# Kernel tuning notes

Measured on AMD Instinct MI355X. Metric: run time of the kernel, lower is better.

The kernel has to match this reference:

```python
import jax, jax.numpy as jnp
import numpy as np

B, C, H, W = 4096, 2, 64, 64
D = 1.0 / (H - 1)  # grid spacing d0 = d1
CLAMP_MIN = -27.6310211159


def fd1_last(f, d):
    # 2nd-order accurate first derivative along last axis, non-periodic.
    c = (f[..., 2:] - f[..., :-2]) / (2.0 * d)
    lo = (-3.0 * f[..., 0:1] + 4.0 * f[..., 1:2] - f[..., 2:3]) / (2.0 * d)
    hi = (3.0 * f[..., -1:] - 4.0 * f[..., -2:-1] + f[..., -3:-2]) / (2.0 * d)
    return jnp.concatenate([lo, c, hi], axis=-1)


def fd2_last(f, d):
    # 2nd-order accurate second derivative along last axis, non-periodic.
    d2 = d * d
    c = (f[..., 2:] - 2.0 * f[..., 1:-1] + f[..., :-2]) / d2
    lo = (2.0 * f[..., 0:1] - 5.0 * f[..., 1:2] + 4.0 * f[..., 2:3] - f[..., 3:4]) / d2
    hi = (2.0 * f[..., -1:] - 5.0 * f[..., -2:-1] + 4.0 * f[..., -3:-2] - f[..., -4:-3]) / d2
    return jnp.concatenate([lo, c, hi], axis=-1)


def fd_axis(f, d, axis, order):
    fn = fd1_last if order == 1 else fd2_last
    if axis == -1 or axis == f.ndim - 1:
        return fn(f, d)
    g = jnp.swapaxes(f, axis, -1)
    return jnp.swapaxes(fn(g, d), axis, -1)


def darcy_source(h, w, r=10.0, w_frac=0.125):
    ww = int(round(w_frac * h))
    f = np.zeros((h, w), dtype=np.float32)
    f[:ww, :ww] = r
    f[-ww:, -ww:] = -r
    return jnp.asarray(f)


def compute_residual(x0):
    # x0: (B, 2, H, W) with channel 0 = pressure p, channel 1 = permeability K
    p, perm = x0[:, 0], x0[:, 1]
    p_d0 = fd_axis(p, D, -2, 1)
    p_d1 = fd_axis(p, D, -1, 1)
    p_d00 = fd_axis(p, D, -2, 2)
    p_d11 = fd_axis(p, D, -1, 2)
    perm_d0 = fd_axis(perm, D, -2, 1)
    perm_d1 = fd_axis(perm, D, -1, 1)

    f_s = darcy_source(H, W)  # (H, W)
    # div(-K grad p) - f  (only diagonal of velocity jacobian is populated)
    eq0 = (-perm * p_d00 - perm_d0 * p_d0) + (-perm * p_d11 - perm_d1 * p_d1) - f_s  # (B,H,W)

    # Neumann boundary residuals on grad p (channel 0 = d/d0, channel 1 = d/d1)
    bc = jnp.zeros((x0.shape[0], 2, H, W), dtype=x0.dtype)
    bc = bc.at[:, 0, 0, :].set(-p_d0[:, 0, :])
    bc = bc.at[:, 0, -1, :].set(p_d0[:, -1, :])
    bc = bc.at[:, 1, :, 0].set(p_d1[:, :, 0])
    bc = bc.at[:, 1, :, -1].set(-p_d1[:, :, -1])

    # b c x y -> b (x y) c  layout, then concat eq0 as an extra channel
    eq0_flat = eq0.reshape(eq0.shape[0], H * W, 1)
    bc_flat = jnp.transpose(bc, (0, 2, 3, 1)).reshape(bc.shape[0], H * W, 2)
    residual = jnp.concatenate([eq0_flat, bc_flat], axis=-1)  # (B, HW, 3)
    return residual.mean(axis=(1, 2))  # (B,)


def darcy_loss(model_out, target, x0_hat, var):
    data_loss = jnp.mean((model_out - target) ** 2)
    r = compute_residual(x0_hat)  # (B,)
    ll = -0.5 * (r ** 2) / var  # gaussian log-likelihood of 0 under N(r, var)
    ll = jnp.maximum(ll, CLAMP_MIN)
    residual_loss = jnp.mean(-ll)
    c_residual = 1.0
    return data_loss + c_residual * residual_loss


def setup_inputs() -> dict:
    key = jax.random.key(0)
    k1, k2, k3, k4 = jax.random.split(key, 4)
    return {
        "model_out": jax.random.normal(k1, (B, C, H, W), dtype=jnp.float32),
        "target": jax.random.normal(k2, (B, C, H, W), dtype=jnp.float32),
        "x0_hat": jax.random.normal(k3, (B, C, H, W), dtype=jnp.float32),
        "var": jax.random.uniform(k4, (B,), dtype=jnp.float32, minval=0.5, maxval=1.5),
    }


def reference(model_out, target, x0_hat, var):
    return darcy_loss(model_out, target, x0_hat, var)
```

## Files before the change

### kernel.cpp

```cpp
#include <hip/hip_runtime.h>


#define NB 4096
#define HW 4096
#define CHW 8192

__device__ __forceinline__ void hderiv2(float v, int j, float& d1, float& d11) {
    constexpr float INV2D = 31.5f, INVD2 = 3969.0f;
    float vm = __shfl(v, (j + 63) & 63);
    float vp = __shfl(v, (j + 1) & 63);
    float v2 = __shfl(v, (j == 0) ? 2 : 61);
    float v3 = __shfl(v, (j == 0) ? 3 : 60);
    d1  = (vp - vm) * INV2D;
    d11 = (vp - 2.0f * v + vm) * INVD2;
    if (j == 0)  { d1 = (-3.0f * v + 4.0f * vp - v2) * INV2D;
                   d11 = (2.0f * v - 5.0f * vp + 4.0f * v2 - v3) * INVD2; }
    if (j == 63) { d1 = ( 3.0f * v - 4.0f * vm + v2) * INV2D;
                   d11 = (2.0f * v - 5.0f * vm + 4.0f * v2 - v3) * INVD2; }
}

__device__ __forceinline__ float hderiv1(float v, int j) {
    constexpr float INV2D = 31.5f;
    float vm = __shfl(v, (j + 63) & 63);
    float vp = __shfl(v, (j + 1) & 63);
    float v2 = __shfl(v, (j == 0) ? 2 : 61);
    float d = (vp - vm) * INV2D;
    if (j == 0)  d = (-3.0f * v + 4.0f * vp - v2) * INV2D;
    if (j == 63) d = ( 3.0f * v - 4.0f * vm + v2) * INV2D;
    return d;
}

__global__ __launch_bounds__(256, 8) void darcy_wave_kernel(
    const float* __restrict__ mo, const float* __restrict__ tg,
    const float* __restrict__ x0, const float* __restrict__ var,
    float* __restrict__ ws_res, float* __restrict__ ws_data)
{
    constexpr float INV2D = 31.5f;
    constexpr float INVD2 = 3969.0f;
    constexpr float CLAMP = 27.6310211159f;

    const int wave = threadIdx.x >> 6;
    const int j    = threadIdx.x & 63;
    const int b    = blockIdx.x * 4 + wave;

    const float*  pb = x0 + (size_t)b * CHW;
    const float*  qb = pb + HW;
    const float4* m4 = (const float4*)(mo + (size_t)b * CHW);
    const float4* g4 = (const float4*)(tg + (size_t)b * CHW);

    float rsum = 0.0f, dsum = 0.0f;

    float pm = pb[j], pc = pb[64 + j], pp = pb[128 + j], pn = pb[192 + j];
    float qm = qb[j], qc = qb[64 + j], qp = qb[128 + j], qn = qb[192 + j];

    {
        float pd1, pd11;
        hderiv2(pm, j, pd1, pd11);
        float qd1 = hderiv1(qm, j);
        float pd0  = (-3.0f * pm + 4.0f * pc - pp) * INV2D;
        float pd00 = (2.0f * pm - 5.0f * pc + 4.0f * pp - pn) * INVD2;
        float qd0  = (-3.0f * qm + 4.0f * qc - qp) * INV2D;
        rsum += -qm * (pd00 + pd11) - qd0 * pd0 - qd1 * pd1 - pd0;
        rsum += (j == 0) ? pd1 : 0.0f;
        rsum -= (j == 63) ? pd1 : 0.0f;
    }

    float s_p60 = 0.0f, s_p61 = 0.0f, s_q61 = 0.0f;

    #pragma unroll 2
    for (int i = 1; i <= 62; ++i) {
        float pn2 = 0.0f, qn2 = 0.0f;
        if (i <= 60) {
            pn2 = pb[((i + 3) << 6) + j];
            qn2 = qb[((i + 3) << 6) + j];
        }
        if (i <= 32) {
            const int k = (i - 1) << 6;
            float4 a = m4[j + k];
            float4 c = g4[j + k];
            float e0 = a.x - c.x, e1 = a.y - c.y, e2 = a.z - c.z, e3 = a.w - c.w;
            dsum += e0 * e0 + e1 * e1 + e2 * e2 + e3 * e3;
        }

        float pd1, pd11;
        hderiv2(pc, j, pd1, pd11);
        float qd1 = hderiv1(qc, j);
        float pd0  = (pp - pm) * INV2D;
        float pd00 = (pp - 2.0f * pc + pm) * INVD2;
        float qd0  = (qp - qm) * INV2D;
        rsum += -qc * (pd00 + pd11) - qd0 * pd0 - qd1 * pd1;
        rsum += (j == 0) ? pd1 : 0.0f;
        rsum -= (j == 63) ? pd1 : 0.0f;

        if (i == 61) s_p60 = pm;
        if (i == 62) { s_p61 = pm; s_q61 = qm; }

        pm = pc; pc = pp; pp = pn; pn = pn2;
        qm = qc; qc = qp; qp = qn; qn = qn2;
    }

    {
        float pd1, pd11;
        hderiv2(pc, j, pd1, pd11);
        float qd1 = hderiv1(qc, j);
        float pd0  = (3.0f * pc - 4.0f * pm + s_p61) * INV2D;
        float pd00 = (2.0f * pc - 5.0f * pm + 4.0f * s_p61 - s_p60) * INVD2;
        float qd0  = (3.0f * qc - 4.0f * qm + s_q61) * INV2D;
        rsum += -qc * (pd00 + pd11) - qd0 * pd0 - qd1 * pd1 + pd0;
        rsum += (j == 0) ? pd1 : 0.0f;
        rsum -= (j == 63) ? pd1 : 0.0f;
    }

    #pragma unroll
    for (int off = 32; off > 0; off >>= 1) {
        rsum += __shfl_down(rsum, off);
        dsum += __shfl_down(dsum, off);
    }
    if (j == 0) {
        const float r = rsum * (1.0f / (64.0f * 64.0f * 3.0f));
        float res = 0.5f * r * r / var[b];
        ws_res[b]  = fminf(res, CLAMP);
        ws_data[b] = dsum;
    }
}

__global__ __launch_bounds__(256) void darcy_final_kernel(
    const float* __restrict__ ws_res, const float* __restrict__ ws_data,
    float* __restrict__ out)
{
    const int t = threadIdx.x;
    double rs = 0.0, ds = 0.0;
    for (int i = t; i < NB; i += 256) {
        rs += (double)ws_res[i];
        ds += (double)ws_data[i];
    }
    #pragma unroll
    for (int off = 32; off > 0; off >>= 1) {
        rs += __shfl_down(rs, off);
        ds += __shfl_down(ds, off);
    }
    __shared__ double red[8];
    const int wid = t >> 6, lane = t & 63;
    if (lane == 0) { red[wid] = rs; red[4 + wid] = ds; }
    __syncthreads();
    if (t == 0) {
        const double R  = red[0] + red[1] + red[2] + red[3];
        const double Dd = red[4] + red[5] + red[6] + red[7];
        out[0] = (float)(Dd / ((double)NB * (double)CHW) + R / (double)NB);
    }
}

extern "C" void kernel_launch(void* const* d_in, const int* in_sizes, int n_in,
                              void* d_out, int out_size, void* d_ws, size_t ws_size,
                              hipStream_t stream) {
    const float* mo  = (const float*)d_in[0];
    const float* tg  = (const float*)d_in[1];
    const float* x0  = (const float*)d_in[2];
    const float* var = (const float*)d_in[3];
    float* out = (float*)d_out;

    float* ws_res  = (float*)d_ws;
    float* ws_data = ws_res + NB;

    darcy_wave_kernel<<<NB / 4, 256, 0, stream>>>(mo, tg, x0, var, ws_res, ws_data);
    darcy_final_kernel<<<1, 256, 0, stream>>>(ws_res, ws_data, out);
}
```

Baseline: 84.90 us.

## Deepen row prefetch with fully unrolled ring buffer and nontemporal loads

Replaces the 4-row sliding window with an 8-entry register ring buffer that prefetches rows 6 ahead, and fully unrolls the 62-iteration loop so the ring indices become compile-time constants. The data-loss loads switch to nontemporal vector loads, and the launch bound drops to 4 waves per EU, which gives each thread more registers. The aim is more memory-level parallelism to hide load latency in this bandwidth-bound pass. The cost is higher register pressure, possibly lower occupancy, and larger code.

```diff
diff --git a/kernel.cpp b/kernel.cpp
--- a/kernel.cpp
+++ b/kernel.cpp
@@ -4,6 +4,8 @@
 #define NB 4096
 #define HW 4096
 #define CHW 8192
+
+typedef float vf4 __attribute__((ext_vector_type(4)));
 
 __device__ __forceinline__ void hderiv2(float v, int j, float& d1, float& d11) {
     constexpr float INV2D = 31.5f, INVD2 = 3969.0f;
@@ -30,57 +32,60 @@
     return d;
 }
 
-__global__ __launch_bounds__(256, 8) void darcy_wave_kernel(
+__global__ __launch_bounds__(256, 4) void darcy_wave_kernel(
     const float* __restrict__ mo, const float* __restrict__ tg,
     const float* __restrict__ x0, const float* __restrict__ var,
-    float* __restrict__ ws_res, float* __restrict__ ws_data)
+    float* __restrict__ ws_res, float* __restrict__ ws_d)
 {
     constexpr float INV2D = 31.5f;
     constexpr float INVD2 = 3969.0f;
     constexpr float CLAMP = 27.6310211159f;
 
-    const int wave = threadIdx.x >> 6;
-    const int j    = threadIdx.x & 63;
-    const int b    = blockIdx.x * 4 + wave;
+    const int wv = threadIdx.x >> 6;
+    const int j  = threadIdx.x & 63;
+    const int b  = blockIdx.x * 4 + wv;
 
-    const float*  pb = x0 + (size_t)b * CHW;
-    const float*  qb = pb + HW;
-    const float4* m4 = (const float4*)(mo + (size_t)b * CHW);
-    const float4* g4 = (const float4*)(tg + (size_t)b * CHW);
+    const float* pb = x0 + (size_t)b * CHW;
+    const float* qb = pb + HW;
+    const vf4*   m4 = (const vf4*)(mo + (size_t)b * CHW);
+    const vf4*   g4 = (const vf4*)(tg + (size_t)b * CHW);
 
     float rsum = 0.0f, dsum = 0.0f;
 
-    float pm = pb[j], pc = pb[64 + j], pp = pb[128 + j], pn = pb[192 + j];
-    float qm = qb[j], qc = qb[64 + j], qp = qb[128 + j], qn = qb[192 + j];
+    float ps[8], qs[8];
+    #pragma unroll
+    for (int k = 0; k < 7; ++k) {
+        ps[k] = pb[(k << 6) + j];
+        qs[k] = qb[(k << 6) + j];
+    }
 
     {
         float pd1, pd11;
-        hderiv2(pm, j, pd1, pd11);
-        float qd1 = hderiv1(qm, j);
-        float pd0  = (-3.0f * pm + 4.0f * pc - pp) * INV2D;
-        float pd00 = (2.0f * pm - 5.0f * pc + 4.0f * pp - pn) * INVD2;
-        float qd0  = (-3.0f * qm + 4.0f * qc - qp) * INV2D;
-        rsum += -qm * (pd00 + pd11) - qd0 * pd0 - qd1 * pd1 - pd0;
+        hderiv2(ps[0], j, pd1, pd11);
+        float qd1 = hderiv1(qs[0], j);
+        float pd0  = (-3.0f * ps[0] + 4.0f * ps[1] - ps[2]) * INV2D;
+        float pd00 = (2.0f * ps[0] - 5.0f * ps[1] + 4.0f * ps[2] - ps[3]) * INVD2;
+        float qd0  = (-3.0f * qs[0] + 4.0f * qs[1] - qs[2]) * INV2D;
+        rsum += -qs[0] * (pd00 + pd11) - qd0 * pd0 - qd1 * pd1 - pd0;
         rsum += (j == 0) ? pd1 : 0.0f;
         rsum -= (j == 63) ? pd1 : 0.0f;
     }
 
-    float s_p60 = 0.0f, s_p61 = 0.0f, s_q61 = 0.0f;
-
-    #pragma unroll 2
+    #pragma unroll
     for (int i = 1; i <= 62; ++i) {
-        float pn2 = 0.0f, qn2 = 0.0f;
-        if (i <= 60) {
-            pn2 = pb[((i + 3) << 6) + j];
-            qn2 = qb[((i + 3) << 6) + j];
+        if (i + 6 <= 63) {
+            ps[(i + 6) & 7] = pb[((i + 6) << 6) + j];
+            qs[(i + 6) & 7] = qb[((i + 6) << 6) + j];
         }
         if (i <= 32) {
-            const int k = (i - 1) << 6;
-            float4 a = m4[j + k];
-            float4 c = g4[j + k];
-            float e0 = a.x - c.x, e1 = a.y - c.y, e2 = a.z - c.z, e3 = a.w - c.w;
-            dsum += e0 * e0 + e1 * e1 + e2 * e2 + e3 * e3;
+            vf4 a = __builtin_nontemporal_load(m4 + ((i - 1) << 6) + j);
+            vf4 c = __builtin_nontemporal_load(g4 + ((i - 1) << 6) + j);
+            vf4 e = a - c;
+            dsum += e.x * e.x + e.y * e.y + e.z * e.z + e.w * e.w;
         }
+
+        const float pm = ps[(i - 1) & 7], pc = ps[i & 7], pp = ps[(i + 1) & 7];
+        const float qm = qs[(i - 1) & 7], qc = qs[i & 7], qp = qs[(i + 1) & 7];
 
         float pd1, pd11;
         hderiv2(pc, j, pd1, pd11);
@@ -91,22 +96,18 @@
         rsum += -qc * (pd00 + pd11) - qd0 * pd0 - qd1 * pd1;
         rsum += (j == 0) ? pd1 : 0.0f;
         rsum -= (j == 63) ? pd1 : 0.0f;
-
-        if (i == 61) s_p60 = pm;
-        if (i == 62) { s_p61 = pm; s_q61 = qm; }
-
-        pm = pc; pc = pp; pp = pn; pn = pn2;
-        qm = qc; qc = qp; qp = qn; qn = qn2;
     }
 
     {
+        const float p63 = ps[7], p62 = ps[6], p61 = ps[5], p60 = ps[4];
+        const float q63 = qs[7], q62 = qs[6], q61 = qs[5];
         float pd1, pd11;
-        hderiv2(pc, j, pd1, pd11);
-        float qd1 = hderiv1(qc, j);
-        float pd0  = (3.0f * pc - 4.0f * pm + s_p61) * INV2D;
-        float pd00 = (2.0f * pc - 5.0f * pm + 4.0f * s_p61 - s_p60) * INVD2;
-        float qd0  = (3.0f * qc - 4.0f * qm + s_q61) * INV2D;
-        rsum += -qc * (pd00 + pd11) - qd0 * pd0 - qd1 * pd1 + pd0;
+        hderiv2(p63, j, pd1, pd11);
+        float qd1 = hderiv1(q63, j);
+        float pd0  = (3.0f * p63 - 4.0f * p62 + p61) * INV2D;
+        float pd00 = (2.0f * p63 - 5.0f * p62 + 4.0f * p61 - p60) * INVD2;
+        float qd0  = (3.0f * q63 - 4.0f * q62 + q61) * INV2D;
+        rsum += -q63 * (pd00 + pd11) - qd0 * pd0 - qd1 * pd1 + pd0;
         rsum += (j == 0) ? pd1 : 0.0f;
         rsum -= (j == 63) ? pd1 : 0.0f;
     }
@@ -119,20 +120,20 @@
     if (j == 0) {
         const float r = rsum * (1.0f / (64.0f * 64.0f * 3.0f));
         float res = 0.5f * r * r / var[b];
-        ws_res[b]  = fminf(res, CLAMP);
-        ws_data[b] = dsum;
+        ws_res[b] = fminf(res, CLAMP);
+        ws_d[b]   = dsum;
     }
 }
 
 __global__ __launch_bounds__(256) void darcy_final_kernel(
-    const float* __restrict__ ws_res, const float* __restrict__ ws_data,
+    const float* __restrict__ ws_res, const float* __restrict__ ws_d,
     float* __restrict__ out)
 {
     const int t = threadIdx.x;
     double rs = 0.0, ds = 0.0;
     for (int i = t; i < NB; i += 256) {
         rs += (double)ws_res[i];
-        ds += (double)ws_data[i];
+        ds += (double)ws_d[i];
     }
     #pragma unroll
     for (int off = 32; off > 0; off >>= 1) {
@@ -159,9 +160,9 @@
     const float* var = (const float*)d_in[3];
     float* out = (float*)d_out;
 
-    float* ws_res  = (float*)d_ws;
-    float* ws_data = ws_res + NB;
+    float* ws_res = (float*)d_ws;
+    float* ws_d   = ws_res + NB;
 
-    darcy_wave_kernel<<<NB / 4, 256, 0, stream>>>(mo, tg, x0, var, ws_res, ws_data);
-    darcy_final_kernel<<<1, 256, 0, stream>>>(ws_res, ws_data, out);
+    darcy_wave_kernel<<<NB / 4, 256, 0, stream>>>(mo, tg, x0, var, ws_res, ws_d);
+    darcy_final_kernel<<<1, 256, 0, stream>>>(ws_res, ws_d, out);
 }
```

Result: faster. 72.81 us (-14.2%).
